# Kernel optimization log

Measured on AMD Instinct MI355X. Metric: run time of the kernel, lower is better.

## Reference

```python
import jax, jax.numpy as jnp
import numpy as np

V, E, H, L, C = 30000, 512, 256, 2, 16  # vocab, embed, lstm hidden, layers, tags
B, S = 32, 512
NH, HD = 2, (2 * H) // 2  # attention heads, head dim


def setup_inputs() -> dict:
    key = jax.random.key(0)
    ks = jax.random.split(key, 16)
    s = 0.05
    return {
        "x": jax.random.randint(ks[0], (B, S), 0, V),
        "labels": jax.random.randint(ks[1], (B, S), 0, C),
        "emb": jax.random.normal(ks[2], (V, E), jnp.float32) * s,
        # stacked LSTM params: [layer, dir, ...]; layer0 in=E=512, layer1 in=2H=512
        "lstm_wih": jax.random.normal(ks[3], (L, 2, 4 * H, E), jnp.float32) * s,
        "lstm_whh": jax.random.normal(ks[4], (L, 2, 4 * H, H), jnp.float32) * s,
        "lstm_bih": jax.random.normal(ks[5], (L, 2, 4 * H), jnp.float32) * s,
        "lstm_bhh": jax.random.normal(ks[6], (L, 2, 4 * H), jnp.float32) * s,
        "in_proj_w": jax.random.normal(ks[7], (3 * 2 * H, 2 * H), jnp.float32) * s,
        "in_proj_b": jax.random.normal(ks[8], (3 * 2 * H,), jnp.float32) * s,
        "out_proj_w": jax.random.normal(ks[9], (2 * H, 2 * H), jnp.float32) * s,
        "out_proj_b": jax.random.normal(ks[10], (2 * H,), jnp.float32) * s,
        "fc_w": jax.random.normal(ks[11], (C, 2 * H), jnp.float32) * s,
        "fc_b": jax.random.normal(ks[12], (C,), jnp.float32) * s,
        "crf_start": jax.random.normal(ks[13], (C,), jnp.float32) * s,
        "crf_end": jax.random.normal(ks[14], (C,), jnp.float32) * s,
        "crf_trans": jax.random.normal(ks[15], (C, C), jnp.float32) * s,
    }


def _lstm_dir(x_sbf, wih, whh, b, reverse):
    # x_sbf: [S, B, F]; PyTorch gate order i, f, g, o
    h0 = jnp.zeros((x_sbf.shape[1], whh.shape[1]), x_sbf.dtype)

    def step(carry, xt):
        h, c = carry
        z = xt @ wih.T + h @ whh.T + b
        i, f, g, o = jnp.split(z, 4, axis=-1)
        c = jax.nn.sigmoid(f) * c + jax.nn.sigmoid(i) * jnp.tanh(g)
        h = jax.nn.sigmoid(o) * jnp.tanh(c)
        return (h, c), h

    _, hs = jax.lax.scan(step, (h0, h0), x_sbf, reverse=reverse)
    return hs  # [S, B, H], aligned to input time order


def _bilstm(x, lstm_wih, lstm_whh, lstm_bih, lstm_bhh):
    # x: [B, S, E] -> [B, S, 2H]; dropout between layers skipped (eval)
    h = jnp.swapaxes(x, 0, 1)  # [S, B, E]
    for l in range(L):
        b_f = lstm_bih[l, 0] + lstm_bhh[l, 0]
        b_b = lstm_bih[l, 1] + lstm_bhh[l, 1]
        fwd = _lstm_dir(h, lstm_wih[l, 0], lstm_whh[l, 0], b_f, False)
        bwd = _lstm_dir(h, lstm_wih[l, 1], lstm_whh[l, 1], b_b, True)
        h = jnp.concatenate([fwd, bwd], axis=-1)  # [S, B, 2H]
    return jnp.swapaxes(h, 0, 1)  # [B, S, 2H]


def _mha(x, in_proj_w, in_proj_b, out_proj_w, out_proj_b):
    # Faithful to the source bug: nn.MultiheadAttention (seq-first) is fed
    # batch-first data, so axis 0 (batch B) is the attention/sequence axis
    # and axis 1 (S) acts as the batch. x: [B, S, 2H]
    qkv = x @ in_proj_w.T + in_proj_b
    q, k, v = jnp.split(qkv, 3, axis=-1)
    q = q.reshape(B, S, NH, HD)
    k = k.reshape(B, S, NH, HD)
    v = v.reshape(B, S, NH, HD)
    scores = jnp.einsum('lshd,mshd->hslm', q, k) / np.sqrt(HD).astype(np.float32)
    attn = jax.nn.softmax(scores, axis=-1)
    out = jnp.einsum('hslm,mshd->lshd', attn, v).reshape(B, S, 2 * H)
    return out @ out_proj_w.T + out_proj_b


def _crf_nll(emissions, tags, crf_start, crf_end, crf_trans):
    # torchcrf log-likelihood, full mask, reduction='sum'; returns -llh
    em = jnp.swapaxes(emissions, 0, 1)   # [S, B, C]
    tg = jnp.swapaxes(tags, 0, 1)        # [S, B]
    bidx = jnp.arange(B)

    # numerator: score of the gold path
    score0 = crf_start[tg[0]] + em[0, bidx, tg[0]]

    def num_step(score, xs):
        em_t, tp, tt = xs
        return score + crf_trans[tp, tt] + em_t[bidx, tt], None

    score, _ = jax.lax.scan(num_step, score0, (em[1:], tg[:-1], tg[1:]))
    score = score + crf_end[tg[-1]]

    # denominator: forward algorithm (logsumexp recurrence)
    alpha0 = crf_start[None, :] + em[0]  # [B, C]

    def fwd_step(alpha, em_t):
        nxt = jax.nn.logsumexp(alpha[:, :, None] + crf_trans[None] + em_t[:, None, :], axis=1)
        return nxt, None

    alpha, _ = jax.lax.scan(fwd_step, alpha0, em[1:])
    logZ = jax.nn.logsumexp(alpha + crf_end[None, :], axis=1)

    llh = jnp.sum(score - logZ)
    return -llh


def reference(x, labels, emb, lstm_wih, lstm_whh, lstm_bih, lstm_bhh,
              in_proj_w, in_proj_b, out_proj_w, out_proj_b,
              fc_w, fc_b, crf_start, crf_end, crf_trans):
    e = emb[x]                                              # [B, S, E]
    h = _bilstm(e, lstm_wih, lstm_whh, lstm_bih, lstm_bhh)  # [B, S, 2H]
    a = _mha(h, in_proj_w, in_proj_b, out_proj_w, out_proj_b)
    logits = a @ fc_w.T + fc_b                              # [B, S, C]
    nll = _crf_nll(logits, labels, crf_start, crf_end, crf_trans)
    return logits, nll
```

## Files before the change

kernel.cpp:

```cpp
#include <hip/hip_runtime.h>
#include <hip/hip_bf16.h>
#include <cstdint>

#define S_ 512
#define B_ 32
#define E_ 512
#define H_ 256
#define C_ 16

typedef float f32x4_t __attribute__((ext_vector_type(4)));
typedef __bf16 bf16x8_t __attribute__((ext_vector_type(8)));

__device__ __forceinline__ float bf2f(unsigned short u) {
    return __uint_as_float(((unsigned int)u) << 16);
}
__device__ __forceinline__ unsigned short f2bf(float f) {
    unsigned int u = __float_as_uint(f);
    unsigned int r = (u + 0x7FFFu + ((u >> 16) & 1u)) >> 16;
    return (unsigned short)r;
}
__device__ __forceinline__ float sigf(float x) { return 1.f / (1.f + __expf(-x)); }
__device__ __forceinline__ float tanhf_fast(float x) {
    float e = __expf(-2.f * fabsf(x));
    float r = (1.f - e) / (1.f + e);
    return x >= 0.f ? r : -r;
}

__global__ __launch_bounds__(128) void embed_gather(
    const int* __restrict__ x, const float* __restrict__ emb, unsigned short* __restrict__ X)
{
    int row = blockIdx.x;
    int s = row >> 5, b = row & 31;
    int idx = x[b * S_ + s];
    float4 v = ((const float4*)(emb + (size_t)idx * E_))[threadIdx.x];
    ushort4 o; o.x = f2bf(v.x); o.y = f2bf(v.y); o.z = f2bf(v.z); o.w = f2bf(v.w);
    ((ushort4*)(X + (size_t)row * E_))[threadIdx.x] = o;
}

__global__ __launch_bounds__(256) void conv_f2b(
    const float* __restrict__ src, unsigned short* __restrict__ dst, int n)
{
    int i = (blockIdx.x * 256 + threadIdx.x) * 4;
    if (i < n) {
        float4 v = *(const float4*)(src + i);
        ushort4 o; o.x = f2bf(v.x); o.y = f2bf(v.y); o.z = f2bf(v.z); o.w = f2bf(v.w);
        *(ushort4*)(dst + i) = o;
    }
}

__global__ __launch_bounds__(256) void zero_ws(unsigned int* __restrict__ p, int n)
{
    int i = blockIdx.x * 256 + threadIdx.x;
    if (i < n) p[i] = 0u;
}

template<int STORE_BF16>
__global__ __launch_bounds__(256) void gemm_bf16(
    const unsigned short* __restrict__ A, const unsigned short* __restrict__ W,
    const float* __restrict__ b1, const float* __restrict__ b2,
    void* __restrict__ Cout, int M, int N, int K)
{
    __shared__ __align__(16) char lds[16384];
    char* asb = lds;
    char* wsb = lds + 8192;
    const int tid = threadIdx.x;
    const int m0 = blockIdx.x * 64, n0 = blockIdx.y * 64;
    const int w = tid >> 6, L = tid & 63;
    const int sr = tid >> 2, sq = tid & 3;
    const int mrow = L & 15, kg = (L >> 4) * 8;
    f32x4_t acc[4];
    #pragma unroll
    for (int ni = 0; ni < 4; ++ni) acc[ni] = f32x4_t{0.f, 0.f, 0.f, 0.f};

    for (int k0 = 0; k0 < K; k0 += 64) {
        uint4 av1 = *(const uint4*)(A + (size_t)(m0 + sr) * K + k0 + sq * 16);
        uint4 av2 = *(const uint4*)(A + (size_t)(m0 + sr) * K + k0 + sq * 16 + 8);
        uint4 wv1 = *(const uint4*)(W + (size_t)(n0 + sr) * K + k0 + sq * 16);
        uint4 wv2 = *(const uint4*)(W + (size_t)(n0 + sr) * K + k0 + sq * 16 + 8);
        __syncthreads();
        int sw = (sr & 7) << 4;
        *(uint4*)(asb + ((sr * 128 + sq * 32) ^ sw))      = av1;
        *(uint4*)(asb + ((sr * 128 + sq * 32 + 16) ^ sw)) = av2;
        *(uint4*)(wsb + ((sr * 128 + sq * 32) ^ sw))      = wv1;
        *(uint4*)(wsb + ((sr * 128 + sq * 32 + 16) ^ sw)) = wv2;
        __syncthreads();
        #pragma unroll
        for (int kb = 0; kb < 2; ++kb) {
            int kl = kb * 32 + kg;
            int ar = w * 16 + mrow;
            bf16x8_t a = *(const bf16x8_t*)(asb + ((ar * 128 + kl * 2) ^ ((ar & 7) << 4)));
            #pragma unroll
            for (int ni = 0; ni < 4; ++ni) {
                int nr = ni * 16 + mrow;
                bf16x8_t b = *(const bf16x8_t*)(wsb + ((nr * 128 + kl * 2) ^ ((nr & 7) << 4)));
                acc[ni] = __builtin_amdgcn_mfma_f32_16x16x32_bf16(a, b, acc[ni], 0, 0, 0);
            }
        }
    }
    #pragma unroll
    for (int ni = 0; ni < 4; ++ni) {
        int n = n0 + ni * 16 + mrow;
        float bb = (b1 ? b1[n] : 0.f) + (b2 ? b2[n] : 0.f);
        #pragma unroll
        for (int r = 0; r < 4; ++r) {
            int m = m0 + w * 16 + (L >> 4) * 4 + r;
            float v = acc[ni][r] + bb;
            size_t off = (size_t)m * N + n;
            if (STORE_BF16) ((unsigned short*)Cout)[off] = f2bf(v);
            else            ((float*)Cout)[off] = v;
        }
    }
}

__global__ __launch_bounds__(256) void lstm_rec_mfma(
    const unsigned short* __restrict__ Zf,
    const unsigned short* __restrict__ Zb,
    const float* __restrict__ whh_l,
    unsigned int* __restrict__ hglob,
    unsigned int* __restrict__ flags,
    unsigned short* __restrict__ Hb)
{
    __shared__ __align__(16) char lds[147456];
    const int tid = threadIdx.x;
    const int d = blockIdx.x >> 2;
    const int p = blockIdx.x & 3;
    const int w = tid >> 6;
    const int L = tid & 63;
    const unsigned short* Z = d ? Zb : Zf;
    unsigned int* hgd = hglob + d * 8192;
    unsigned int* fld = flags + d * 4;

    {
        int rloc = tid >> 2, q = tid & 3;
        for (int rr = 0; rr < 256; rr += 64) {
            int r = rr + rloc;
            int g = r >> 6, u = r & 63;
            const float* src = whh_l + ((size_t)d * 1024 + g * 256 + p * 64 + u) * 256;
            #pragma unroll
            for (int i = 0; i < 16; ++i) {
                int c4 = (i * 4 + q) * 4;
                float4 w4 = *(const float4*)(src + c4);
                ushort4 b4;
                b4.x = f2bf(w4.x); b4.y = f2bf(w4.y); b4.z = f2bf(w4.z); b4.w = f2bf(w4.w);
                int byt = ((r * 256 + c4) * 2) ^ ((r & 7) << 4);
                *(ushort4*)(lds + byt) = b4;
            }
        }
    }
    char* hz = lds + 131072;
    const int sb = tid >> 3, sj = tid & 7;
    {
        int byt = (sb * 512 + p * 128 + sj * 16) ^ ((sb & 7) << 4);
        uint4 zz; zz.x = 0; zz.y = 0; zz.z = 0; zz.w = 0;
        *(uint4*)(hz + byt) = zz;
    }
    float cst[8] = {0.f, 0.f, 0.f, 0.f, 0.f, 0.f, 0.f, 0.f};
    const int mrow = L & 15;
    const int kg = (L >> 4) * 8;
    const int ug = p * 64 + w * 16 + mrow;
    __syncthreads();

    for (int tt = 0; tt < 512; ++tt) {
        const int t = d ? (511 - tt) : tt;

        unsigned short zxv[4][8];
        #pragma unroll
        for (int g = 0; g < 4; ++g)
            #pragma unroll
            for (int j = 0; j < 8; ++j) {
                int b = (j >> 2) * 16 + (L >> 4) * 4 + (j & 3);
                zxv[g][j] = Z[((size_t)t * 32 + b) * 1024 + g * 256 + ug];
            }

        f32x4_t acc[4][2];
        #pragma unroll
        for (int g = 0; g < 4; ++g) {
            acc[g][0] = f32x4_t{0.f, 0.f, 0.f, 0.f};
            acc[g][1] = f32x4_t{0.f, 0.f, 0.f, 0.f};
        }

        #pragma unroll
        for (int kk = 0; kk < 2; ++kk) {
            int k0 = (2 * p + kk) * 32 + kg;
            bf16x8_t a0 = *(const bf16x8_t*)(hz + ((mrow * 512 + k0 * 2) ^ ((mrow & 7) << 4)));
            bf16x8_t a1 = *(const bf16x8_t*)(hz + (((mrow + 16) * 512 + k0 * 2) ^ ((mrow & 7) << 4)));
            #pragma unroll
            for (int g = 0; g < 4; ++g) {
                int n = g * 64 + w * 16 + mrow;
                bf16x8_t bf = *(const bf16x8_t*)(lds + ((n * 512 + k0 * 2) ^ ((n & 7) << 4)));
                acc[g][0] = __builtin_amdgcn_mfma_f32_16x16x32_bf16(a0, bf, acc[g][0], 0, 0, 0);
                acc[g][1] = __builtin_amdgcn_mfma_f32_16x16x32_bf16(a1, bf, acc[g][1], 0, 0, 0);
            }
        }

        if (tt > 0) {
            #pragma unroll
            for (int qq = 1; qq < 4; ++qq) {
                int q = (p + qq) & 3;
                while (__hip_atomic_load(fld + q, __ATOMIC_RELAXED, __HIP_MEMORY_SCOPE_AGENT)
                       < (unsigned)tt) { }
            }
        }
        {
            const unsigned int* hgp = hgd + ((tt + 1) & 1) * 4096;
            #pragma unroll
            for (int qq = 1; qq < 4; ++qq) {
                int q = (p + qq) & 3;
                const unsigned int* sp = hgp + sb * 128 + q * 32 + sj * 4;
                unsigned int v0 = __hip_atomic_load(sp + 0, __ATOMIC_RELAXED, __HIP_MEMORY_SCOPE_AGENT);
                unsigned int v1 = __hip_atomic_load(sp + 1, __ATOMIC_RELAXED, __HIP_MEMORY_SCOPE_AGENT);
                unsigned int v2 = __hip_atomic_load(sp + 2, __ATOMIC_RELAXED, __HIP_MEMORY_SCOPE_AGENT);
                unsigned int v3 = __hip_atomic_load(sp + 3, __ATOMIC_RELAXED, __HIP_MEMORY_SCOPE_AGENT);
                int byt = (sb * 512 + q * 128 + sj * 16) ^ ((sb & 7) << 4);
                uint4 v; v.x = v0; v.y = v1; v.z = v2; v.w = v3;
                *(uint4*)(hz + byt) = v;
            }
        }
        __syncthreads();

        #pragma unroll
        for (int qq = 1; qq < 4; ++qq) {
            int q = (p + qq) & 3;
            #pragma unroll
            for (int kk = 0; kk < 2; ++kk) {
                int k0 = (2 * q + kk) * 32 + kg;
                bf16x8_t a0 = *(const bf16x8_t*)(hz + ((mrow * 512 + k0 * 2) ^ ((mrow & 7) << 4)));
                bf16x8_t a1 = *(const bf16x8_t*)(hz + (((mrow + 16) * 512 + k0 * 2) ^ ((mrow & 7) << 4)));
                #pragma unroll
                for (int g = 0; g < 4; ++g) {
                    int n = g * 64 + w * 16 + mrow;
                    bf16x8_t bf = *(const bf16x8_t*)(lds + ((n * 512 + k0 * 2) ^ ((n & 7) << 4)));
                    acc[g][0] = __builtin_amdgcn_mfma_f32_16x16x32_bf16(a0, bf, acc[g][0], 0, 0, 0);
                    acc[g][1] = __builtin_amdgcn_mfma_f32_16x16x32_bf16(a1, bf, acc[g][1], 0, 0, 0);
                }
            }
        }

        #pragma unroll
        for (int mh = 0; mh < 2; ++mh)
            #pragma unroll
            for (int r = 0; r < 4; ++r) {
                int j = mh * 4 + r;
                float iv = sigf(acc[0][mh][r] + bf2f(zxv[0][j]));
                float fv = sigf(acc[1][mh][r] + bf2f(zxv[1][j]));
                float gv = tanhf_fast(acc[2][mh][r] + bf2f(zxv[2][j]));
                float ov = sigf(acc[3][mh][r] + bf2f(zxv[3][j]));
                cst[j] = fv * cst[j] + iv * gv;
                float hh = ov * tanhf_fast(cst[j]);
                int b = mh * 16 + (L >> 4) * 4 + r;
                *(unsigned short*)(hz + ((b * 512 + ug * 2) ^ ((b & 7) << 4))) = f2bf(hh);
            }
        __syncthreads();

        {
            unsigned int* hgp = hgd + (tt & 1) * 4096;
            int byt = (sb * 512 + p * 128 + sj * 16) ^ ((sb & 7) << 4);
            uint4 v = *(const uint4*)(hz + byt);
            unsigned int* dp = hgp + sb * 128 + p * 32 + sj * 4;
            __hip_atomic_store(dp + 0, v.x, __ATOMIC_RELAXED, __HIP_MEMORY_SCOPE_AGENT);
            __hip_atomic_store(dp + 1, v.y, __ATOMIC_RELAXED, __HIP_MEMORY_SCOPE_AGENT);
            __hip_atomic_store(dp + 2, v.z, __ATOMIC_RELAXED, __HIP_MEMORY_SCOPE_AGENT);
            __hip_atomic_store(dp + 3, v.w, __ATOMIC_RELAXED, __HIP_MEMORY_SCOPE_AGENT);
            *(uint4*)(Hb + ((size_t)t * 32 + sb) * 512 + d * 256 + p * 64 + sj * 8) = v;
        }
        __syncthreads();

        if (tid == 0)
            __hip_atomic_store(fld + p, (unsigned)(tt + 1), __ATOMIC_RELAXED, __HIP_MEMORY_SCOPE_AGENT);
    }
}

__global__ __launch_bounds__(256) void attn_fused(
    const unsigned short* __restrict__ qkv, unsigned short* __restrict__ outp)
{
    int s = blockIdx.x & 511;
    int h = blockIdx.x >> 9;
    __shared__ float qs[32][260];
    __shared__ float ks[32][260];
    __shared__ float vs[32][260];
    __shared__ float sc[32][36];
    int tid = threadIdx.x;
    for (int it = 0; it < 32; ++it) {
        const unsigned short* base = qkv + ((size_t)s * 32 + it) * 1536 + h * 256 + tid;
        qs[it][tid] = bf2f(base[0]);
        ks[it][tid] = bf2f(base[512]);
        vs[it][tid] = bf2f(base[1024]);
    }
    __syncthreads();
    int l = tid >> 3, m0 = (tid & 7) * 4;
    float a0 = 0, a1 = 0, a2 = 0, a3 = 0;
    for (int dd = 0; dd < 256; dd += 4) {
        float4 q4 = *(const float4*)&qs[l][dd];
        float4 k0v = *(const float4*)&ks[m0 + 0][dd];
        float4 k1v = *(const float4*)&ks[m0 + 1][dd];
        float4 k2v = *(const float4*)&ks[m0 + 2][dd];
        float4 k3v = *(const float4*)&ks[m0 + 3][dd];
        a0 += q4.x * k0v.x + q4.y * k0v.y + q4.z * k0v.z + q4.w * k0v.w;
        a1 += q4.x * k1v.x + q4.y * k1v.y + q4.z * k1v.z + q4.w * k1v.w;
        a2 += q4.x * k2v.x + q4.y * k2v.y + q4.z * k2v.z + q4.w * k2v.w;
        a3 += q4.x * k3v.x + q4.y * k3v.y + q4.z * k3v.z + q4.w * k3v.w;
    }
    sc[l][m0 + 0] = a0 * 0.0625f;
    sc[l][m0 + 1] = a1 * 0.0625f;
    sc[l][m0 + 2] = a2 * 0.0625f;
    sc[l][m0 + 3] = a3 * 0.0625f;
    __syncthreads();
    if (tid < 32) {
        float mx = -1e30f;
        for (int m = 0; m < 32; ++m) mx = fmaxf(mx, sc[tid][m]);
        float pr[32]; float sm = 0.f;
        for (int m = 0; m < 32; ++m) { pr[m] = __expf(sc[tid][m] - mx); sm += pr[m]; }
        float inv = 1.f / sm;
        for (int m = 0; m < 32; ++m) sc[tid][m] = pr[m] * inv;
    }
    __syncthreads();
    int l2 = tid >> 3, d0 = (tid & 7) * 32;
    float o[32] = {};
    for (int m = 0; m < 32; ++m) {
        float aw = sc[l2][m];
        #pragma unroll
        for (int dd = 0; dd < 32; dd += 4) {
            float4 v4 = *(const float4*)&vs[m][d0 + dd];
            o[dd] += aw * v4.x; o[dd + 1] += aw * v4.y; o[dd + 2] += aw * v4.z; o[dd + 3] += aw * v4.w;
        }
    }
    unsigned short* ob = outp + ((size_t)s * 32 + l2) * 512 + h * 256 + d0;
    #pragma unroll
    for (int dd = 0; dd < 32; dd += 4) {
        ushort4 pv;
        pv.x = f2bf(o[dd]); pv.y = f2bf(o[dd + 1]); pv.z = f2bf(o[dd + 2]); pv.w = f2bf(o[dd + 3]);
        *(ushort4*)(ob + dd) = pv;
    }
}

__global__ __launch_bounds__(256) void fc_logits(
    const float* __restrict__ A, const float* __restrict__ fcw, const float* __restrict__ fcb,
    float* __restrict__ outp)
{
    __shared__ float wsm[16][516];
    int tid = threadIdx.x;
    for (int idx = tid; idx < 8192; idx += 256) wsm[idx >> 9][idx & 511] = fcw[idx];
    __syncthreads();
    int r = blockIdx.x * 16 + (tid >> 4);
    int c = tid & 15;
    const float* ar = A + (size_t)r * 512;
    float acc = 0.f;
    for (int k = 0; k < 512; k += 4) {
        float4 a4 = *(const float4*)(ar + k);
        float4 w4 = *(const float4*)&wsm[c][k];
        acc += a4.x * w4.x + a4.y * w4.y + a4.z * w4.z + a4.w * w4.w;
    }
    int s = r >> 5, b = r & 31;
    outp[(size_t)b * 8192 + s * 16 + c] = acc + fcb[c];
}

__global__ __launch_bounds__(256) void crf_forward(
    const float* __restrict__ em, const int* __restrict__ labels,
    const float* __restrict__ cs, const float* __restrict__ ce, const float* __restrict__ ct,
    float* __restrict__ res)
{
    int b = blockIdx.x;
    int tid = threadIdx.x;
    int jj = tid >> 4, ii = tid & 15;
    __shared__ float trans[16][17];
    __shared__ float alpha[2][16];
    __shared__ float red[256];
    trans[tid >> 4][tid & 15] = ct[tid & 255];
    const float* emb_ = em + (size_t)b * 8192;
    const int* tg = labels + b * 512;
    float part = 0.f;
    for (int t = tid; t < 512; t += 256) {
        int cur = tg[t];
        part += emb_[t * 16 + cur] + (t == 0 ? cs[cur] : ct[tg[t - 1] * 16 + cur]);
    }
    red[tid] = part;
    if (tid < 16) alpha[0][tid] = cs[tid] + emb_[tid];
    __syncthreads();
    for (int off = 128; off > 0; off >>= 1) {
        if (tid < off) red[tid] += red[tid + off];
        __syncthreads();
    }
    for (int t = 1; t < 512; ++t) {
        int p = t & 1;
        float v = alpha[p ^ 1][ii] + trans[ii][jj];
        float mx = v;
        mx = fmaxf(mx, __shfl_xor(mx, 1));
        mx = fmaxf(mx, __shfl_xor(mx, 2));
        mx = fmaxf(mx, __shfl_xor(mx, 4));
        mx = fmaxf(mx, __shfl_xor(mx, 8));
        float e = __expf(v - mx);
        e += __shfl_xor(e, 1); e += __shfl_xor(e, 2); e += __shfl_xor(e, 4); e += __shfl_xor(e, 8);
        if (ii == 0) alpha[p][jj] = mx + __logf(e) + emb_[t * 16 + jj];
        __syncthreads();
    }
    if (tid == 0) {
        float mx = -1e30f;
        for (int c2 = 0; c2 < 16; ++c2) mx = fmaxf(mx, alpha[1][c2] + ce[c2]);
        float sm = 0.f;
        for (int c2 = 0; c2 < 16; ++c2) sm += __expf(alpha[1][c2] + ce[c2] - mx);
        float logZ = mx + __logf(sm);
        float score = red[0] + ce[tg[511]];
        res[b] = logZ - score;
    }
}

__global__ void crf_final(const float* __restrict__ res, float* __restrict__ nll)
{
    if (threadIdx.x == 0) {
        float s2 = 0.f;
        for (int b = 0; b < 32; ++b) s2 += res[b];
        nll[0] = s2;
    }
}

extern "C" void kernel_launch(void* const* d_in, const int* in_sizes, int n_in,
                              void* d_out, int out_size, void* d_ws, size_t ws_size,
                              hipStream_t stream)
{
    const int* x      = (const int*)d_in[0];
    const int* labels = (const int*)d_in[1];
    const float* emb  = (const float*)d_in[2];
    const float* wih  = (const float*)d_in[3];
    const float* whh  = (const float*)d_in[4];
    const float* bih  = (const float*)d_in[5];
    const float* bhh  = (const float*)d_in[6];
    const float* inw  = (const float*)d_in[7];
    const float* inb  = (const float*)d_in[8];
    const float* opw  = (const float*)d_in[9];
    const float* opb  = (const float*)d_in[10];
    const float* fcw  = (const float*)d_in[11];
    const float* fcb  = (const float*)d_in[12];
    const float* cs   = (const float*)d_in[13];
    const float* ce   = (const float*)d_in[14];
    const float* ct   = (const float*)d_in[15];
    float* out = (float*)d_out;

    char* ws = (char*)d_ws;
    const size_t MiB = 1ull << 20;
    unsigned short* Xb     = (unsigned short*)(ws);
    unsigned short* attnO  = (unsigned short*)(ws);
    unsigned int*   hgf    = (unsigned int*)(ws);
    unsigned short* H0b    = (unsigned short*)(ws + 16 * MiB);
    float*          res    = (float*)(ws + 16 * MiB);
    unsigned short* H1b    = (unsigned short*)(ws + 32 * MiB);
    unsigned short* wihb   = (unsigned short*)(ws + 32 * MiB);
    unsigned short* opwb   = (unsigned short*)(ws + 32 * MiB);
    unsigned short* Zfb    = (unsigned short*)(ws + 48 * MiB);
    unsigned short* inwb   = (unsigned short*)(ws + 48 * MiB);
    float*          OPout  = (float*)(ws + 48 * MiB);
    unsigned short* Zbb    = (unsigned short*)(ws + 80 * MiB);
    unsigned short* qkv    = (unsigned short*)(ws + 80 * MiB);

    embed_gather<<<16384, 128, 0, stream>>>(x, emb, Xb);

    conv_f2b<<<2048, 256, 0, stream>>>(wih, wihb, 2097152);

    for (int l = 0; l < 2; ++l) {
        const unsigned short* Ain = l ? H0b : Xb;
        unsigned short* Ho        = l ? H1b : H0b;
        for (int dd = 0; dd < 2; ++dd) {
            gemm_bf16<1><<<dim3(256, 16), 256, 0, stream>>>(
                Ain, wihb + (size_t)(l * 2 + dd) * 524288,
                bih + (l * 2 + dd) * 1024, bhh + (l * 2 + dd) * 1024,
                dd ? (void*)Zbb : (void*)Zfb, 16384, 1024, 512);
        }
        zero_ws<<<65, 256, 0, stream>>>(hgf, 16392);
        lstm_rec_mfma<<<8, 256, 0, stream>>>(
            Zfb, Zbb, whh + (size_t)l * 524288, hgf, hgf + 16384, Ho);
    }

    conv_f2b<<<768, 256, 0, stream>>>(inw, inwb, 786432);
    gemm_bf16<1><<<dim3(256, 24), 256, 0, stream>>>(H1b, inwb, inb, nullptr, (void*)qkv, 16384, 1536, 512);
    conv_f2b<<<256, 256, 0, stream>>>(opw, opwb, 262144);
    attn_fused<<<1024, 256, 0, stream>>>(qkv, attnO);
    gemm_bf16<0><<<dim3(256, 8), 256, 0, stream>>>(attnO, opwb, opb, nullptr, (void*)OPout, 16384, 512, 512);

    fc_logits<<<1024, 256, 0, stream>>>(OPout, fcw, fcb, out);

    crf_forward<<<32, 256, 0, stream>>>(out, labels, cs, ce, ct, res);
    crf_final<<<1, 64, 0, stream>>>(res, out + 262144);

    (void)in_sizes; (void)n_in; (void)out_size; (void)ws_size;
}
```

Measured before the change: 5.167 ms.

## Restructure LSTM recurrence into 2 blocks per direction with tagged h exchange

Replaces the 4-block-per-direction LSTM recurrence with 2 blocks of 512 threads per direction. W_hh is held in registers as bf16 instead of LDS. Cross-block hidden-state exchange now uses 64-bit words that pack the data with a step tag, which removes the separate flag polling and the extra barrier. Weight conversions are hoisted and the workspace layout is reorganised. This targets the per-step synchronisation latency of the serial recurrence, at the cost of heavy register pressure and reliance on the tag protocol across layers.

```diff
diff --git a/kernel.cpp b/kernel.cpp
--- a/kernel.cpp
+++ b/kernel.cpp
@@ -112,53 +112,36 @@
     }
 }
 
-__global__ __launch_bounds__(256) void lstm_rec_mfma(
+__global__ __launch_bounds__(512) void lstm_rec2(
     const unsigned short* __restrict__ Zf,
     const unsigned short* __restrict__ Zb,
-    const float* __restrict__ whh_l,
-    unsigned int* __restrict__ hglob,
-    unsigned int* __restrict__ flags,
+    const unsigned short* __restrict__ whhb,
+    unsigned long long* __restrict__ hglob,
+    unsigned int tagbase,
     unsigned short* __restrict__ Hb)
 {
-    __shared__ __align__(16) char lds[147456];
+    __shared__ __align__(16) char lds[16384];
     const int tid = threadIdx.x;
-    const int d = blockIdx.x >> 2;
-    const int p = blockIdx.x & 3;
-    const int w = tid >> 6;
-    const int L = tid & 63;
+    const int d = blockIdx.x >> 1;
+    const int p = blockIdx.x & 1;
+    const int w = tid >> 6, L = tid & 63;
+    const int mrow = L & 15;
+    const int kg8 = (L >> 4) * 8;
+    const int swz = (mrow & 7) << 4;
+    const int u = p * 128 + w * 16 + mrow;
     const unsigned short* Z = d ? Zb : Zf;
-    unsigned int* hgd = hglob + d * 8192;
-    unsigned int* fld = flags + d * 4;
-
-    {
-        int rloc = tid >> 2, q = tid & 3;
-        for (int rr = 0; rr < 256; rr += 64) {
-            int r = rr + rloc;
-            int g = r >> 6, u = r & 63;
-            const float* src = whh_l + ((size_t)d * 1024 + g * 256 + p * 64 + u) * 256;
-            #pragma unroll
-            for (int i = 0; i < 16; ++i) {
-                int c4 = (i * 4 + q) * 4;
-                float4 w4 = *(const float4*)(src + c4);
-                ushort4 b4;
-                b4.x = f2bf(w4.x); b4.y = f2bf(w4.y); b4.z = f2bf(w4.z); b4.w = f2bf(w4.w);
-                int byt = ((r * 256 + c4) * 2) ^ ((r & 7) << 4);
-                *(ushort4*)(lds + byt) = b4;
-            }
-        }
-    }
-    char* hz = lds + 131072;
-    const int sb = tid >> 3, sj = tid & 7;
-    {
-        int byt = (sb * 512 + p * 128 + sj * 16) ^ ((sb & 7) << 4);
-        uint4 zz; zz.x = 0; zz.y = 0; zz.z = 0; zz.w = 0;
-        *(uint4*)(hz + byt) = zz;
-    }
+    unsigned long long* hgd = hglob + (size_t)d * 8192;
+
+    bf16x8_t wreg[4][8];
+    #pragma unroll
+    for (int g = 0; g < 4; ++g)
+        #pragma unroll
+        for (int j = 0; j < 8; ++j) {
+            int kt = (j < 4) ? (p * 4 + j) : ((1 - p) * 4 + (j - 4));
+            wreg[g][j] = *(const bf16x8_t*)(
+                whhb + ((size_t)d * 1024 + g * 256 + u) * 256 + kt * 32 + kg8);
+        }
     float cst[8] = {0.f, 0.f, 0.f, 0.f, 0.f, 0.f, 0.f, 0.f};
-    const int mrow = L & 15;
-    const int kg = (L >> 4) * 8;
-    const int ug = p * 64 + w * 16 + mrow;
-    __syncthreads();
 
     for (int tt = 0; tt < 512; ++tt) {
         const int t = d ? (511 - tt) : tt;
@@ -169,7 +152,7 @@
             #pragma unroll
             for (int j = 0; j < 8; ++j) {
                 int b = (j >> 2) * 16 + (L >> 4) * 4 + (j & 3);
-                zxv[g][j] = Z[((size_t)t * 32 + b) * 1024 + g * 256 + ug];
+                zxv[g][j] = Z[((size_t)t * 32 + b) * 1024 + g * 256 + u];
             }
 
         f32x4_t acc[4][2];
@@ -179,63 +162,70 @@
             acc[g][1] = f32x4_t{0.f, 0.f, 0.f, 0.f};
         }
 
-        #pragma unroll
-        for (int kk = 0; kk < 2; ++kk) {
-            int k0 = (2 * p + kk) * 32 + kg;
-            bf16x8_t a0 = *(const bf16x8_t*)(hz + ((mrow * 512 + k0 * 2) ^ ((mrow & 7) << 4)));
-            bf16x8_t a1 = *(const bf16x8_t*)(hz + (((mrow + 16) * 512 + k0 * 2) ^ ((mrow & 7) << 4)));
-            #pragma unroll
-            for (int g = 0; g < 4; ++g) {
-                int n = g * 64 + w * 16 + mrow;
-                bf16x8_t bf = *(const bf16x8_t*)(lds + ((n * 512 + k0 * 2) ^ ((n & 7) << 4)));
-                acc[g][0] = __builtin_amdgcn_mfma_f32_16x16x32_bf16(a0, bf, acc[g][0], 0, 0, 0);
-                acc[g][1] = __builtin_amdgcn_mfma_f32_16x16x32_bf16(a1, bf, acc[g][1], 0, 0, 0);
-            }
-        }
-
         if (tt > 0) {
             #pragma unroll
-            for (int qq = 1; qq < 4; ++qq) {
-                int q = (p + qq) & 3;
-                while (__hip_atomic_load(fld + q, __ATOMIC_RELAXED, __HIP_MEMORY_SCOPE_AGENT)
-                       < (unsigned)tt) { }
-            }
-        }
-        {
-            const unsigned int* hgp = hgd + ((tt + 1) & 1) * 4096;
-            #pragma unroll
-            for (int qq = 1; qq < 4; ++qq) {
-                int q = (p + qq) & 3;
-                const unsigned int* sp = hgp + sb * 128 + q * 32 + sj * 4;
-                unsigned int v0 = __hip_atomic_load(sp + 0, __ATOMIC_RELAXED, __HIP_MEMORY_SCOPE_AGENT);
-                unsigned int v1 = __hip_atomic_load(sp + 1, __ATOMIC_RELAXED, __HIP_MEMORY_SCOPE_AGENT);
-                unsigned int v2 = __hip_atomic_load(sp + 2, __ATOMIC_RELAXED, __HIP_MEMORY_SCOPE_AGENT);
-                unsigned int v3 = __hip_atomic_load(sp + 3, __ATOMIC_RELAXED, __HIP_MEMORY_SCOPE_AGENT);
-                int byt = (sb * 512 + q * 128 + sj * 16) ^ ((sb & 7) << 4);
-                uint4 v; v.x = v0; v.y = v1; v.z = v2; v.w = v3;
-                *(uint4*)(hz + byt) = v;
-            }
-        }
-        __syncthreads();
-
-        #pragma unroll
-        for (int qq = 1; qq < 4; ++qq) {
-            int q = (p + qq) & 3;
-            #pragma unroll
-            for (int kk = 0; kk < 2; ++kk) {
-                int k0 = (2 * q + kk) * 32 + kg;
-                bf16x8_t a0 = *(const bf16x8_t*)(hz + ((mrow * 512 + k0 * 2) ^ ((mrow & 7) << 4)));
-                bf16x8_t a1 = *(const bf16x8_t*)(hz + (((mrow + 16) * 512 + k0 * 2) ^ ((mrow & 7) << 4)));
+            for (int kk = 0; kk < 4; ++kk) {
+                int kb = (p * 4 + kk) * 32 + kg8;
+                bf16x8_t a0 = *(const bf16x8_t*)(lds + ((mrow * 512 + kb * 2) ^ swz));
+                bf16x8_t a1 = *(const bf16x8_t*)(lds + (((mrow + 16) * 512 + kb * 2) ^ swz));
                 #pragma unroll
                 for (int g = 0; g < 4; ++g) {
-                    int n = g * 64 + w * 16 + mrow;
-                    bf16x8_t bf = *(const bf16x8_t*)(lds + ((n * 512 + k0 * 2) ^ ((n & 7) << 4)));
-                    acc[g][0] = __builtin_amdgcn_mfma_f32_16x16x32_bf16(a0, bf, acc[g][0], 0, 0, 0);
-                    acc[g][1] = __builtin_amdgcn_mfma_f32_16x16x32_bf16(a1, bf, acc[g][1], 0, 0, 0);
-                }
-            }
-        }
-
+                    acc[g][0] = __builtin_amdgcn_mfma_f32_16x16x32_bf16(a0, wreg[g][kk], acc[g][0], 0, 0, 0);
+                    acc[g][1] = __builtin_amdgcn_mfma_f32_16x16x32_bf16(a1, wreg[g][kk], acc[g][1], 0, 0, 0);
+                }
+            }
+            {
+                unsigned long long* slot = hgd + (size_t)((tt + 1) & 1) * 4096;
+                const int pb = (1 - p) * 64;
+                const unsigned int expt = tagbase + (unsigned int)tt;
+                int l0 = tid, l1 = 512 + tid, l2 = 1024 + tid, l3 = 1536 + tid;
+                unsigned long long* a0p = slot + (l0 >> 6) * 128 + pb + (l0 & 63);
+                unsigned long long* a1p = slot + (l1 >> 6) * 128 + pb + (l1 & 63);
+                unsigned long long* a2p = slot + (l2 >> 6) * 128 + pb + (l2 & 63);
+                unsigned long long* a3p = slot + (l3 >> 6) * 128 + pb + (l3 & 63);
+                unsigned long long v0, v1, v2, v3;
+                for (;;) {
+                    v0 = __hip_atomic_load(a0p, __ATOMIC_RELAXED, __HIP_MEMORY_SCOPE_AGENT);
+                    v1 = __hip_atomic_load(a1p, __ATOMIC_RELAXED, __HIP_MEMORY_SCOPE_AGENT);
+                    v2 = __hip_atomic_load(a2p, __ATOMIC_RELAXED, __HIP_MEMORY_SCOPE_AGENT);
+                    v3 = __hip_atomic_load(a3p, __ATOMIC_RELAXED, __HIP_MEMORY_SCOPE_AGENT);
+                    if (((unsigned int)v0 == expt) & ((unsigned int)v1 == expt) &
+                        ((unsigned int)v2 == expt) & ((unsigned int)v3 == expt)) break;
+                    __builtin_amdgcn_s_sleep(1);
+                }
+                int ub2 = (1 - p) * 128;
+                {
+                    int b = l0 >> 6, uu = ub2 + (l0 & 63) * 2;
+                    *(unsigned int*)(lds + ((b * 512 + uu * 2) ^ ((b & 7) << 4))) = (unsigned int)(v0 >> 32);
+                }
+                {
+                    int b = l1 >> 6, uu = ub2 + (l1 & 63) * 2;
+                    *(unsigned int*)(lds + ((b * 512 + uu * 2) ^ ((b & 7) << 4))) = (unsigned int)(v1 >> 32);
+                }
+                {
+                    int b = l2 >> 6, uu = ub2 + (l2 & 63) * 2;
+                    *(unsigned int*)(lds + ((b * 512 + uu * 2) ^ ((b & 7) << 4))) = (unsigned int)(v2 >> 32);
+                }
+                {
+                    int b = l3 >> 6, uu = ub2 + (l3 & 63) * 2;
+                    *(unsigned int*)(lds + ((b * 512 + uu * 2) ^ ((b & 7) << 4))) = (unsigned int)(v3 >> 32);
+                }
+            }
+            __syncthreads();
+            #pragma unroll
+            for (int kk = 0; kk < 4; ++kk) {
+                int kb = ((1 - p) * 4 + kk) * 32 + kg8;
+                bf16x8_t a0 = *(const bf16x8_t*)(lds + ((mrow * 512 + kb * 2) ^ swz));
+                bf16x8_t a1 = *(const bf16x8_t*)(lds + (((mrow + 16) * 512 + kb * 2) ^ swz));
+                #pragma unroll
+                for (int g = 0; g < 4; ++g) {
+                    acc[g][0] = __builtin_amdgcn_mfma_f32_16x16x32_bf16(a0, wreg[g][4 + kk], acc[g][0], 0, 0, 0);
+                    acc[g][1] = __builtin_amdgcn_mfma_f32_16x16x32_bf16(a1, wreg[g][4 + kk], acc[g][1], 0, 0, 0);
+                }
+            }
+        }
+
+        float hh[8];
         #pragma unroll
         for (int mh = 0; mh < 2; ++mh)
             #pragma unroll
@@ -246,27 +236,30 @@
                 float gv = tanhf_fast(acc[2][mh][r] + bf2f(zxv[2][j]));
                 float ov = sigf(acc[3][mh][r] + bf2f(zxv[3][j]));
                 cst[j] = fv * cst[j] + iv * gv;
-                float hh = ov * tanhf_fast(cst[j]);
-                int b = mh * 16 + (L >> 4) * 4 + r;
-                *(unsigned short*)(hz + ((b * 512 + ug * 2) ^ ((b & 7) << 4))) = f2bf(hh);
-            }
+                hh[j] = ov * tanhf_fast(cst[j]);
+            }
+
+        {
+            unsigned long long* oslot = hgd + (size_t)(tt & 1) * 4096;
+            const int up = p * 64 + w * 8 + (mrow >> 1);
+            const int ue = u & ~1;
+            const unsigned long long tagw = (unsigned long long)(tagbase + (unsigned int)tt + 1u);
+            #pragma unroll
+            for (int j = 0; j < 8; ++j) {
+                float ph = __shfl_xor(hh[j], 1);
+                unsigned int mine = f2bf(hh[j]), othr = f2bf(ph);
+                unsigned int pair = (L & 1) ? ((mine << 16) | othr) : ((othr << 16) | mine);
+                if ((L & 1) == (j >> 2)) {
+                    int b = (j >> 2) * 16 + (L >> 4) * 4 + (j & 3);
+                    __hip_atomic_store(oslot + b * 128 + up,
+                                       ((unsigned long long)pair << 32) | tagw,
+                                       __ATOMIC_RELAXED, __HIP_MEMORY_SCOPE_AGENT);
+                    *(unsigned int*)(lds + ((b * 512 + ue * 2) ^ ((b & 7) << 4))) = pair;
+                    *(unsigned int*)(Hb + ((size_t)t * 32 + b) * 512 + d * 256 + ue) = pair;
+                }
+            }
+        }
         __syncthreads();
-
-        {
-            unsigned int* hgp = hgd + (tt & 1) * 4096;
-            int byt = (sb * 512 + p * 128 + sj * 16) ^ ((sb & 7) << 4);
-            uint4 v = *(const uint4*)(hz + byt);
-            unsigned int* dp = hgp + sb * 128 + p * 32 + sj * 4;
-            __hip_atomic_store(dp + 0, v.x, __ATOMIC_RELAXED, __HIP_MEMORY_SCOPE_AGENT);
-            __hip_atomic_store(dp + 1, v.y, __ATOMIC_RELAXED, __HIP_MEMORY_SCOPE_AGENT);
-            __hip_atomic_store(dp + 2, v.z, __ATOMIC_RELAXED, __HIP_MEMORY_SCOPE_AGENT);
-            __hip_atomic_store(dp + 3, v.w, __ATOMIC_RELAXED, __HIP_MEMORY_SCOPE_AGENT);
-            *(uint4*)(Hb + ((size_t)t * 32 + sb) * 512 + d * 256 + p * 64 + sj * 8) = v;
-        }
-        __syncthreads();
-
-        if (tid == 0)
-            __hip_atomic_store(fld + p, (unsigned)(tt + 1), __ATOMIC_RELAXED, __HIP_MEMORY_SCOPE_AGENT);
     }
 }
 
@@ -437,23 +430,27 @@
 
     char* ws = (char*)d_ws;
     const size_t MiB = 1ull << 20;
-    unsigned short* Xb     = (unsigned short*)(ws);
-    unsigned short* attnO  = (unsigned short*)(ws);
-    unsigned int*   hgf    = (unsigned int*)(ws);
-    unsigned short* H0b    = (unsigned short*)(ws + 16 * MiB);
-    float*          res    = (float*)(ws + 16 * MiB);
-    unsigned short* H1b    = (unsigned short*)(ws + 32 * MiB);
-    unsigned short* wihb   = (unsigned short*)(ws + 32 * MiB);
-    unsigned short* opwb   = (unsigned short*)(ws + 32 * MiB);
-    unsigned short* Zfb    = (unsigned short*)(ws + 48 * MiB);
-    unsigned short* inwb   = (unsigned short*)(ws + 48 * MiB);
-    float*          OPout  = (float*)(ws + 48 * MiB);
-    unsigned short* Zbb    = (unsigned short*)(ws + 80 * MiB);
-    unsigned short* qkv    = (unsigned short*)(ws + 80 * MiB);
+    unsigned short* Xb    = (unsigned short*)(ws);
+    unsigned short* attnO = (unsigned short*)(ws);
+    unsigned short* H0b   = (unsigned short*)(ws + 16 * MiB);
+    float*          OPout = (float*)(ws + 16 * MiB);
+    float*          res   = (float*)(ws + 16 * MiB);
+    unsigned short* H1b   = (unsigned short*)(ws + 32 * MiB);
+    unsigned short* Zfb   = (unsigned short*)(ws + 48 * MiB);
+    unsigned short* qkv   = (unsigned short*)(ws + 48 * MiB);
+    unsigned short* Zbb   = (unsigned short*)(ws + 80 * MiB);
+    unsigned short* wihb  = (unsigned short*)(ws + 112 * MiB);
+    unsigned short* whhb  = (unsigned short*)(ws + 116 * MiB);
+    unsigned short* inwb  = (unsigned short*)(ws + 118 * MiB);
+    unsigned short* opwb  = (unsigned short*)(ws + 119 * MiB + 512 * 1024);
+    unsigned long long* hg = (unsigned long long*)(ws + 120 * MiB);
 
     embed_gather<<<16384, 128, 0, stream>>>(x, emb, Xb);
-
     conv_f2b<<<2048, 256, 0, stream>>>(wih, wihb, 2097152);
+    conv_f2b<<<1024, 256, 0, stream>>>(whh, whhb, 1048576);
+    conv_f2b<<<768, 256, 0, stream>>>(inw, inwb, 786432);
+    conv_f2b<<<256, 256, 0, stream>>>(opw, opwb, 262144);
+    zero_ws<<<128, 256, 0, stream>>>((unsigned int*)hg, 32768);
 
     for (int l = 0; l < 2; ++l) {
         const unsigned short* Ain = l ? H0b : Xb;
@@ -464,14 +461,11 @@
                 bih + (l * 2 + dd) * 1024, bhh + (l * 2 + dd) * 1024,
                 dd ? (void*)Zbb : (void*)Zfb, 16384, 1024, 512);
         }
-        zero_ws<<<65, 256, 0, stream>>>(hgf, 16392);
-        lstm_rec_mfma<<<8, 256, 0, stream>>>(
-            Zfb, Zbb, whh + (size_t)l * 524288, hgf, hgf + 16384, Ho);
-    }
-
-    conv_f2b<<<768, 256, 0, stream>>>(inw, inwb, 786432);
+        lstm_rec2<<<4, 512, 0, stream>>>(
+            Zfb, Zbb, whhb + (size_t)l * 524288, hg, (unsigned int)(l * 512), Ho);
+    }
+
     gemm_bf16<1><<<dim3(256, 24), 256, 0, stream>>>(H1b, inwb, inb, nullptr, (void*)qkv, 16384, 1536, 512);
-    conv_f2b<<<256, 256, 0, stream>>>(opw, opwb, 262144);
     attn_fused<<<1024, 256, 0, stream>>>(qkv, attnO);
     gemm_bf16<0><<<dim3(256, 8), 256, 0, stream>>>(attnO, opwb, opb, nullptr, (void*)OPout, 16384, 512, 512);
 
```

Result: slower. 11.23 ms (+117.3%).
